# Performance work log

Hardware: AMD Instinct MI355X
Metric: run time of the kernel (lower is better)

The kernel has to match this reference:

```python
import jax, jax.numpy as jnp
import numpy as np

B, N, NS, D, H = 32, 4096, 16, 512, 8
DH = D // H          # dims_per_head = 64
DFF = 4 * D          # ff_mlp hidden
SCALE = DH ** -0.5
EPS = 1e-8           # slot-attention renorm eps
LN_EPS = 1e-5        # torch LayerNorm default
ITERS = 3


def layer_norm(x, g, b):
    mu = jnp.mean(x, axis=-1, keepdims=True)
    var = jnp.mean((x - mu) ** 2, axis=-1, keepdims=True)
    return (x - mu) * jax.lax.rsqrt(var + LN_EPS) * g + b


def setup_inputs() -> dict:
    key = jax.random.key(0)
    ks = jax.random.split(key, 8)
    s = 0.02
    return {
        "inputs": jax.random.normal(ks[0], (B, N, D), jnp.float32),
        "conditioning": jax.random.normal(ks[1], (B, NS, D), jnp.float32),
        # norm_input
        "ln_in_g": jnp.ones((D,), jnp.float32),
        "ln_in_b": jnp.zeros((D,), jnp.float32),
        # projections (no bias: use_projection_bias=False)
        "Wk": jax.random.normal(ks[2], (D, D), jnp.float32) * s,
        "Wv": jax.random.normal(ks[3], (D, D), jnp.float32) * s,
        "Wq": jax.random.normal(ks[4], (D, D), jnp.float32) * s,
        "Wo": jax.random.normal(ks[5], (D, D), jnp.float32) * s,
        # norm_slots / norm_slots_ff_mlp
        "ln_s_g": jnp.ones((D,), jnp.float32),
        "ln_s_b": jnp.zeros((D,), jnp.float32),
        "ln_f_g": jnp.ones((D,), jnp.float32),
        "ln_f_b": jnp.zeros((D,), jnp.float32),
        # ff_mlp: Linear(D,4D) -> ReLU -> Linear(4D,D)
        "W1": jax.random.normal(ks[6], (D, DFF), jnp.float32) * s,
        "b1": jnp.zeros((DFF,), jnp.float32),
        "W2": jax.random.normal(ks[7], (DFF, D), jnp.float32) * s,
        "b2": jnp.zeros((D,), jnp.float32),
    }


def reference(inputs, conditioning, ln_in_g, ln_in_b, Wk, Wv, Wq, Wo,
              ln_s_g, ln_s_b, ln_f_g, ln_f_b, W1, b1, W2, b2):
    b = inputs.shape[0]
    x = layer_norm(inputs, ln_in_g, ln_in_b)                 # [b, n, D]
    k = (x @ Wk.T).reshape(b, N, H, DH)                      # [b, n, h, dh]
    v = (x @ Wv.T).reshape(b, N, H, DH)

    slots = conditioning
    attn_mean = None
    for _ in range(ITERS):
        slots_prev = slots
        s = layer_norm(slots, ln_s_g, ln_s_b)
        q = (s @ Wq.T).reshape(b, NS, H, DH)                 # [b, ns, h, dh]
        dots = jnp.einsum("bihd,bjhd->bihj", q, k) * SCALE   # [b, ns, h, n]
        # softmax over flattened (slots, heads) axis, per input location j
        attn = jax.nn.softmax(dots.reshape(b, NS * H, N), axis=1)
        attn = attn.reshape(b, NS, H, N)
        attn_before = attn
        attn = attn + EPS
        attn = attn / jnp.sum(attn, axis=-1, keepdims=True)  # renorm over j
        updates = jnp.einsum("bjhd,bihj->bihd", v, attn)     # [b, ns, h, dh]
        updates = updates.reshape(b, NS, D)
        slots = updates @ Wo.T + slots_prev                  # to_o + residual
        slots_prev_ff = slots
        s2 = layer_norm(slots, ln_f_g, ln_f_b)
        s2 = jax.nn.relu(s2 @ W1 + b1) @ W2 + b2             # ff_mlp
        slots = s2 + slots_prev_ff
        attn_mean = jnp.mean(attn_before, axis=2)            # [b, ns, n]
    return slots, attn_mean
```

## Files before the change

kernel.cpp:

```cpp
#include <hip/hip_runtime.h>
#include <cstdint>
#include <cstddef>

typedef __attribute__((ext_vector_type(8))) short short8;
typedef __attribute__((ext_vector_type(4))) short short4v;
typedef __attribute__((ext_vector_type(8))) __bf16 bf16x8;
typedef __attribute__((ext_vector_type(4))) float f32x4;
typedef unsigned short u16;

static constexpr int Bb = 32, Nn = 4096, NSs = 16, Dd = 512, Hh = 8, DFF = 2048;
static constexpr float SCALE = 0.125f;
static constexpr float EPSR  = 1e-8f;
static constexpr float LN_EPS = 1e-5f;

__device__ __forceinline__ u16 f2b(float x) {
  union { float f; uint32_t u; } a; a.f = x;
  uint32_t r = a.u + 0x7fffu + ((a.u >> 16) & 1u);
  return (u16)(r >> 16);
}

__device__ __forceinline__ f32x4 mfma16(short8 a, short8 b, f32x4 c) {
  return __builtin_amdgcn_mfma_f32_16x16x32_bf16(
      __builtin_bit_cast(bf16x8, a), __builtin_bit_cast(bf16x8, b), c, 0, 0, 0);
}

__device__ __forceinline__ void gload16(const u16* g, u16* l) {
  __builtin_amdgcn_global_load_lds(
      (const __attribute__((address_space(1))) void*)g,
      (__attribute__((address_space(3))) void*)l, 16, 0, 0);
}

__global__ __launch_bounds__(256) void ln_rows(const float* __restrict__ src,
    const float* __restrict__ g, const float* __restrict__ bt,
    u16* __restrict__ dst, int R) {
  int row = blockIdx.x * 4 + (threadIdx.x >> 6);
  if (row >= R) return;
  int lane = threadIdx.x & 63;
  const float* p = src + (size_t)row * Dd + lane * 8;
  float4 u0 = *(const float4*)p;
  float4 u1 = *(const float4*)(p + 4);
  float x[8] = {u0.x,u0.y,u0.z,u0.w,u1.x,u1.y,u1.z,u1.w};
  float s = 0.f, s2 = 0.f;
#pragma unroll
  for (int e = 0; e < 8; ++e) { s += x[e]; s2 += x[e]*x[e]; }
#pragma unroll
  for (int m = 1; m < 64; m <<= 1) { s += __shfl_xor(s, m); s2 += __shfl_xor(s2, m); }
  float mean = s * (1.f/512.f);
  float var  = s2 * (1.f/512.f) - mean*mean;
  float rstd = rsqrtf(var + LN_EPS);
  union { u16 o[8]; short8 v; } ou;
#pragma unroll
  for (int e = 0; e < 8; ++e)
    ou.o[e] = f2b((x[e]-mean)*rstd*g[lane*8+e] + bt[lane*8+e]);
  *(short8*)(dst + (size_t)row * Dd + lane * 8) = ou.v;
}

__global__ __launch_bounds__(256, 2) void gemm_kv(const u16* __restrict__ A,
    const u16* __restrict__ Bk, const u16* __restrict__ Bv,
    u16* __restrict__ Ck, u16* __restrict__ CvT) {
  __shared__ u16 lA[2][128*32];
  __shared__ u16 lK[2][128*32];
  __shared__ u16 lV[2][128*32];
  const int tid = threadIdx.x, lane = tid & 63, wid = tid >> 6;
  const int wr = wid >> 1, wc = wid & 1;
  const int n  = blockIdx.y * 4 + blockIdx.x;
  const int orig = (n & 7) * 512 + (n >> 3);
  const int bm = (orig >> 2) * 128, bn = (orig & 3) * 128;
  const size_t BN = (size_t)Bb * Nn;
  f32x4 ak[4][4] = {};
  f32x4 av[4][4] = {};
  const int srow = wid*16 + (lane >> 2);
  const int scol = ((lane & 3) ^ ((lane >> 3) & 3)) * 8;
  const u16* Ap = A  + (size_t)(bm + srow) * Dd + scol;
  const u16* Kp = Bk + (size_t)(bn + srow) * Dd + scol;
  const u16* Vp = Bv + (size_t)(bn + srow) * Dd + scol;
  const int ldb = wid * 512;
  const int li = lane & 15, lk = lane >> 4;
  const int csw = (lk ^ ((li >> 1) & 3)) * 8;
#define KV_STAGE(buf, k0) do { \
    gload16(Ap + (k0), &lA[buf][ldb]); \
    gload16(Ap + (size_t)64*Dd + (k0), &lA[buf][ldb + 2048]); \
    gload16(Kp + (k0), &lK[buf][ldb]); \
    gload16(Kp + (size_t)64*Dd + (k0), &lK[buf][ldb + 2048]); \
    gload16(Vp + (k0), &lV[buf][ldb]); \
    gload16(Vp + (size_t)64*Dd + (k0), &lV[buf][ldb + 2048]); \
  } while (0)
  KV_STAGE(0, 0);
  int cur = 0;
  for (int t = 0; t < 16; ++t) {
    if (t < 15) {
      KV_STAGE(cur ^ 1, (t + 1) * 32);
      asm volatile("s_waitcnt vmcnt(6)" ::: "memory");
    } else {
      asm volatile("s_waitcnt vmcnt(0)" ::: "memory");
    }
    __builtin_amdgcn_sched_barrier(0);
    __builtin_amdgcn_s_barrier();
    __builtin_amdgcn_sched_barrier(0);
    short8 af[4], kf[4], vf[4];
#pragma unroll
    for (int m = 0; m < 4; ++m)
      af[m] = *(const short8*)&lA[cur][(wr*64 + m*16 + li)*32 + csw];
#pragma unroll
    for (int nn2 = 0; nn2 < 4; ++nn2) {
      kf[nn2] = *(const short8*)&lK[cur][(wc*64 + nn2*16 + li)*32 + csw];
      vf[nn2] = *(const short8*)&lV[cur][(wc*64 + nn2*16 + li)*32 + csw];
    }
    __builtin_amdgcn_s_setprio(1);
#pragma unroll
    for (int m = 0; m < 4; ++m)
#pragma unroll
      for (int nn2 = 0; nn2 < 4; ++nn2) {
        ak[m][nn2] = mfma16(af[m], kf[nn2], ak[m][nn2]);
        av[m][nn2] = mfma16(af[m], vf[nn2], av[m][nn2]);
      }
    __builtin_amdgcn_s_setprio(0);
    __builtin_amdgcn_sched_barrier(0);
    __builtin_amdgcn_s_barrier();
    __builtin_amdgcn_sched_barrier(0);
    cur ^= 1;
  }
#undef KV_STAGE
  const int lr = lk * 4;
#pragma unroll
  for (int m = 0; m < 4; ++m)
#pragma unroll
    for (int nn2 = 0; nn2 < 4; ++nn2) {
      int row = bm + wr*64 + m*16 + lr;
      int col = bn + wc*64 + nn2*16 + li;
      f32x4 vk = ak[m][nn2];
#pragma unroll
      for (int r = 0; r < 4; ++r)
        Ck[(size_t)(row + r) * Dd + col] = f2b(vk[r]);
      f32x4 vv = av[m][nn2];
      union { u16 o[4]; short4v v4; } ou;
#pragma unroll
      for (int r = 0; r < 4; ++r) ou.o[r] = f2b(vv[r]);
      *(short4v*)&CvT[(size_t)col * BN + row] = ou.v4;
    }
}

template<int EP>
__global__ __launch_bounds__(256) void gemm64(const u16* __restrict__ A,
    const u16* __restrict__ Bw, void* __restrict__ Cp,
    const float* __restrict__ bias, const float* __restrict__ res,
    int N, int K) {
  __shared__ u16 lA[2][64*32];
  __shared__ u16 lB[2][64*32];
  const int tid = threadIdx.x, lane = tid & 63, wid = tid >> 6;
  const int wr = wid >> 1, wc = wid & 1;
  const int bm = blockIdx.y * 64, bn = blockIdx.x * 64;
  f32x4 acc[2][2] = {};
  const int srow = wid*16 + (lane >> 2);
  const int scol = ((lane & 3) ^ ((lane >> 3) & 3)) * 8;
  const u16* Ap = A + (size_t)(bm + srow) * K + scol;
  const u16* Bp = Bw + (size_t)(bn + srow) * K + scol;
  const int ldb = wid * 512;
  const int li = lane & 15, lk = lane >> 4;
  const int csw = (lk ^ ((li >> 1) & 3)) * 8;
  const int nsteps = K >> 5;
  gload16(Ap, &lA[0][ldb]);
  gload16(Bp, &lB[0][ldb]);
  int cur = 0;
  for (int t = 0; t < nsteps; ++t) {
    if (t + 1 < nsteps) {
      const int k0 = (t + 1) * 32;
      gload16(Ap + k0, &lA[cur ^ 1][ldb]);
      gload16(Bp + k0, &lB[cur ^ 1][ldb]);
      asm volatile("s_waitcnt vmcnt(2)" ::: "memory");
    } else {
      asm volatile("s_waitcnt vmcnt(0)" ::: "memory");
    }
    __builtin_amdgcn_sched_barrier(0);
    __builtin_amdgcn_s_barrier();
    __builtin_amdgcn_sched_barrier(0);
    short8 af[2], bf[2];
#pragma unroll
    for (int m = 0; m < 2; ++m)
      af[m] = *(const short8*)&lA[cur][(wr*32 + m*16 + li)*32 + csw];
#pragma unroll
    for (int nn2 = 0; nn2 < 2; ++nn2)
      bf[nn2] = *(const short8*)&lB[cur][(wc*32 + nn2*16 + li)*32 + csw];
    __builtin_amdgcn_s_setprio(1);
#pragma unroll
    for (int m = 0; m < 2; ++m)
#pragma unroll
      for (int nn2 = 0; nn2 < 2; ++nn2)
        acc[m][nn2] = mfma16(af[m], bf[nn2], acc[m][nn2]);
    __builtin_amdgcn_s_setprio(0);
    __builtin_amdgcn_sched_barrier(0);
    __builtin_amdgcn_s_barrier();
    __builtin_amdgcn_sched_barrier(0);
    cur ^= 1;
  }
  const int lr = lk * 4;
#pragma unroll
  for (int m = 0; m < 2; ++m)
#pragma unroll
    for (int nn2 = 0; nn2 < 2; ++nn2) {
      int row = bm + wr*32 + m*16 + lr;
      int col = bn + wc*32 + nn2*16 + li;
      f32x4 v = acc[m][nn2];
#pragma unroll
      for (int r = 0; r < 4; ++r) {
        size_t off = (size_t)(row + r) * N + col;
        float x = v[r];
        if constexpr (EP == 0) ((u16*)Cp)[off] = f2b(x);
        else if constexpr (EP == 1) ((float*)Cp)[off] = x + res[off];
        else if constexpr (EP == 2) { x += bias[col]; ((u16*)Cp)[off] = f2b(x > 0.f ? x : 0.f); }
        else ((float*)Cp)[off] = x + bias[col] + res[off];
      }
    }
}

__global__ __launch_bounds__(256) void attn_a(const u16* __restrict__ q,
    const u16* __restrict__ kk, u16* __restrict__ attnb,
    float* __restrict__ rowsum, float* __restrict__ attn_mean) {
  const int jt = blockIdx.x, b = blockIdx.y;
  const int tid = threadIdx.x, lane = tid & 63, wid = tid >> 6;
  __shared__ float sc[64][129];
  __shared__ float red[4][64];
  const int li = lane & 15, lk = lane >> 4;
#pragma unroll
  for (int hh = 0; hh < 2; ++hh) {
    const int h = wid * 2 + hh;
    const u16* qb = q + (((size_t)b*16 + li)*8 + h)*64 + lk*8;
    short8 a0 = *(const short8*)qb;
    short8 a1 = *(const short8*)(qb + 32);
#pragma unroll
    for (int n = 0; n < 4; ++n) {
      const u16* kb = kk + ((size_t)b*Nn + jt*64 + n*16 + li)*Dd + h*64 + lk*8;
      f32x4 acc = {};
      acc = mfma16(a0, *(const short8*)kb, acc);
      acc = mfma16(a1, *(const short8*)(kb + 32), acc);
#pragma unroll
      for (int r = 0; r < 4; ++r)
        sc[n*16 + li][(lk*4 + r)*8 + h] = acc[r] * SCALE;
    }
  }
  __syncthreads();
  const int jl = tid & 63, qt = tid >> 6;
  float mx = -1e30f;
#pragma unroll
  for (int e = 0; e < 32; ++e) mx = fmaxf(mx, sc[jl][qt*32 + e]);
  red[qt][jl] = mx;
  __syncthreads();
  float M = fmaxf(fmaxf(red[0][jl], red[1][jl]), fmaxf(red[2][jl], red[3][jl]));
  __syncthreads();
  float s = 0.f;
#pragma unroll
  for (int e = 0; e < 32; ++e) {
    float ev = __expf(sc[jl][qt*32 + e] - M);
    sc[jl][qt*32 + e] = ev; s += ev;
  }
  red[qt][jl] = s;
  __syncthreads();
  float S = red[0][jl] + red[1][jl] + red[2][jl] + red[3][jl];
  float inv = 1.f / S;
#pragma unroll
  for (int e = 0; e < 32; ++e)
    sc[jl][qt*32 + e] = sc[jl][qt*32 + e] * inv + EPSR;
  __syncthreads();
  if (tid < 128) {
    float rs = 0.f;
    for (int j2 = 0; j2 < 64; ++j2) rs += sc[j2][tid];
    atomicAdd(&rowsum[b*128 + tid], rs);
  }
#pragma unroll
  for (int e = 0; e < 32; ++e) {
    int r = qt*32 + e;
    attnb[((size_t)b*128 + r)*Nn + jt*64 + jl] = f2b(sc[jl][r]);
  }
  if (attn_mean != nullptr && tid < 64) {
    for (int i = 0; i < 16; ++i) {
      float sm = 0.f;
#pragma unroll
      for (int h = 0; h < 8; ++h) sm += sc[tid][i*8 + h];
      attn_mean[((size_t)b*16 + i)*Nn + jt*64 + tid] = sm * 0.125f - EPSR;
    }
  }
}

__global__ __launch_bounds__(256) void attn_b(const u16* __restrict__ attnb,
    const u16* __restrict__ vT, float* __restrict__ Tpart) {
  const int h = blockIdx.x, js = blockIdx.y, b = blockIdx.z;
  const int lane = threadIdx.x & 63, wid = threadIdx.x >> 6;
  const int li = lane & 15, lk = lane >> 4;
  const size_t BN = (size_t)Bb * Nn;
  const int j0 = js * 1024;
  const u16* Ap = attnb + ((size_t)b*128 + li*8 + h)*Nn + j0 + lk*8;
  const u16* Bp = vT + (size_t)(h*64 + wid*16 + li)*BN + (size_t)b*Nn + j0 + lk*8;
  f32x4 acc[4] = {};
  for (int k0 = 0; k0 < 1024; k0 += 128) {
#pragma unroll
    for (int e = 0; e < 4; ++e)
      acc[e] = mfma16(*(const short8*)(Ap + k0 + e*32),
                      *(const short8*)(Bp + k0 + e*32), acc[e]);
  }
  float* Tout = Tpart + ((((size_t)js * Bb + b) * 8 + h) * 16) * 64;
#pragma unroll
  for (int r = 0; r < 4; ++r) {
    int i = lk*4 + r;
    float t = acc[0][r] + acc[1][r] + acc[2][r] + acc[3][r];
    Tout[(size_t)i * 64 + wid*16 + li] = t;
  }
}

__global__ void upd_c(const float* __restrict__ Tpart,
    const float* __restrict__ rs, u16* __restrict__ updb) {
  int idx = blockIdx.x * 256 + threadIdx.x;
  int o = idx & 511, bi = idx >> 9;
  int b = bi >> 4, i = bi & 15;
  int h = o >> 6, d = o & 63;
  size_t base = (((size_t)b * 8 + h) * 16 + i) * 64 + d;
  const size_t stride = (size_t)Bb * 8 * 16 * 64;
  float t = Tpart[base] + Tpart[base + stride]
          + Tpart[base + 2*stride] + Tpart[base + 3*stride];
  updb[idx] = f2b(t / rs[b * 128 + i * 8 + h]);
}

__global__ void cvt_w(const float* __restrict__ s, u16* __restrict__ d, int n) {
  int i = blockIdx.x*256 + threadIdx.x;
  if (i < n) d[i] = f2b(s[i]);
}
__global__ __launch_bounds__(256) void tr_cvt(const float* __restrict__ s,
    u16* __restrict__ d, int R, int C) {
  __shared__ u16 t[32][33];
  const int c0 = blockIdx.x*32, r0 = blockIdx.y*32;
  const int tr = threadIdx.x >> 3, tc4 = (threadIdx.x & 7)*4;
  float4 v = *(const float4*)&s[(size_t)(r0+tr)*C + c0 + tc4];
  t[tr][tc4+0] = f2b(v.x); t[tr][tc4+1] = f2b(v.y);
  t[tr][tc4+2] = f2b(v.z); t[tr][tc4+3] = f2b(v.w);
  __syncthreads();
  const int oc = threadIdx.x >> 3, or4 = (threadIdx.x & 7)*4;
  union { u16 o[4]; short4v v4; } ou;
#pragma unroll
  for (int e = 0; e < 4; ++e) ou.o[e] = t[or4+e][oc];
  *(short4v*)&d[(size_t)(c0+oc)*R + r0 + or4] = ou.v4;
}
__global__ void copy_f32v4(const float* __restrict__ s, float* __restrict__ d, int n4) {
  int i = blockIdx.x*256 + threadIdx.x;
  if (i < n4) ((float4*)d)[i] = ((const float4*)s)[i];
}

extern "C" void kernel_launch(void* const* d_in, const int* in_sizes, int n_in,
                              void* d_out, int out_size, void* d_ws, size_t ws_size,
                              hipStream_t stream) {
  (void)in_sizes; (void)n_in; (void)out_size; (void)ws_size;
  const float* inputs  = (const float*)d_in[0];
  const float* cond    = (const float*)d_in[1];
  const float* ln_in_g = (const float*)d_in[2];
  const float* ln_in_b = (const float*)d_in[3];
  const float* Wk = (const float*)d_in[4];
  const float* Wv = (const float*)d_in[5];
  const float* Wq = (const float*)d_in[6];
  const float* Wo = (const float*)d_in[7];
  const float* ln_s_g = (const float*)d_in[8];
  const float* ln_s_b = (const float*)d_in[9];
  const float* ln_f_g = (const float*)d_in[10];
  const float* ln_f_b = (const float*)d_in[11];
  const float* W1 = (const float*)d_in[12];
  const float* b1 = (const float*)d_in[13];
  const float* W2 = (const float*)d_in[14];
  const float* b2 = (const float*)d_in[15];
  float* out_slots = (float*)d_out;
  float* out_amean = (float*)d_out + (size_t)Bb*NSs*Dd;

  char* w = (char*)d_ws;
  auto alloc = [&](size_t bytes) {
    char* p = w; w += (bytes + 255) & ~(size_t)255; return p;
  };
  u16*  xn    = (u16*)alloc((size_t)Bb*Nn*Dd*2);
  u16*  kbuf  = (u16*)alloc((size_t)Bb*Nn*Dd*2);
  u16*  vT    = (u16*)alloc((size_t)Bb*Nn*Dd*2);
  u16*  attnb = (u16*)alloc((size_t)Bb*128*Nn*2);
  float* Tpart = (float*)alloc((size_t)4*Bb*8*16*64*4);
  float* slots = (float*)alloc((size_t)Bb*NSs*Dd*4);
  u16*  qb    = (u16*)alloc((size_t)Bb*NSs*Dd*2);
  u16*  snb   = (u16*)alloc((size_t)Bb*NSs*Dd*2);
  u16*  s2nb  = (u16*)alloc((size_t)Bb*NSs*Dd*2);
  u16*  h1b   = (u16*)alloc((size_t)Bb*NSs*DFF*2);
  u16*  updb  = (u16*)alloc((size_t)Bb*NSs*Dd*2);
  float* rowsum = (float*)alloc((size_t)Bb*128*3*4);
  u16*  wkb = (u16*)alloc(262144*2);
  u16*  wvb = (u16*)alloc(262144*2);
  u16*  wqb = (u16*)alloc(262144*2);
  u16*  wob = (u16*)alloc(262144*2);
  u16*  w1t = (u16*)alloc((size_t)1048576*2);
  u16*  w2t = (u16*)alloc((size_t)1048576*2);

  cvt_w<<<1024, 256, 0, stream>>>(Wk, wkb, 262144);
  cvt_w<<<1024, 256, 0, stream>>>(Wv, wvb, 262144);
  cvt_w<<<1024, 256, 0, stream>>>(Wq, wqb, 262144);
  cvt_w<<<1024, 256, 0, stream>>>(Wo, wob, 262144);
  tr_cvt<<<dim3(64, 16), 256, 0, stream>>>(W1, w1t, 512, 2048);
  tr_cvt<<<dim3(16, 64), 256, 0, stream>>>(W2, w2t, 2048, 512);
  copy_f32v4<<<256, 256, 0, stream>>>(cond, slots, 65536);
  (void)hipMemsetAsync(rowsum, 0, (size_t)Bb*128*3*4, stream);
  ln_rows<<<Bb*Nn/4, 256, 0, stream>>>(inputs, ln_in_g, ln_in_b, xn, Bb*Nn);
  gemm_kv<<<dim3(4, Bb*Nn/128), 256, 0, stream>>>(xn, wkb, wvb, kbuf, vT);

  for (int it = 0; it < 3; ++it) {
    float* rsp = rowsum + (size_t)it * Bb * 128;
    ln_rows<<<128, 256, 0, stream>>>(slots, ln_s_g, ln_s_b, snb, Bb*NSs);
    gemm64<0><<<dim3(8, 8), 256, 0, stream>>>(snb, wqb, qb, nullptr, nullptr, 512, 512);
    attn_a<<<dim3(Nn/64, Bb), 256, 0, stream>>>(qb, kbuf, attnb, rsp,
                                                it == 2 ? out_amean : nullptr);
    attn_b<<<dim3(Hh, 4, Bb), 256, 0, stream>>>(attnb, vT, Tpart);
    upd_c<<<1024, 256, 0, stream>>>(Tpart, rsp, updb);
    gemm64<1><<<dim3(8, 8), 256, 0, stream>>>(updb, wob, slots, nullptr, slots, 512, 512);
    ln_rows<<<128, 256, 0, stream>>>(slots, ln_f_g, ln_f_b, s2nb, Bb*NSs);
    gemm64<2><<<dim3(32, 8), 256, 0, stream>>>(s2nb, w1t, h1b, b1, nullptr, 2048, 512);
    gemm64<3><<<dim3(8, 8), 256, 0, stream>>>(h1b, w2t, slots, b2, slots, 512, 2048);
  }
  copy_f32v4<<<256, 256, 0, stream>>>(slots, out_slots, 65536);
}
```

Measured before the change: 705.9 us.

## Enlarge K/V projection GEMM tiles to 256 rows with 512 threads and BK=64

The fused K/V projection GEMM now uses 512-thread blocks covering 256 rows of normalized input by 128 columns of both K and V. The K-step is 64 with a new XOR swizzle, and the prefetch distance grows to two stages. Each block reuses its weight tiles across twice as many rows, and there are half as many barriers per K. In exchange the block needs much more LDS (about 128 KB double-buffered), which can limit occupancy, and the grid is reshaped to 2048 one-dimensional blocks.

```diff
diff --git a/kernel.cpp b/kernel.cpp
--- a/kernel.cpp
+++ b/kernel.cpp
@@ -55,69 +55,81 @@
   *(short8*)(dst + (size_t)row * Dd + lane * 8) = ou.v;
 }
 
-__global__ __launch_bounds__(256, 2) void gemm_kv(const u16* __restrict__ A,
+__global__ __launch_bounds__(512, 2) void gemm_kv(const u16* __restrict__ A,
     const u16* __restrict__ Bk, const u16* __restrict__ Bv,
     u16* __restrict__ Ck, u16* __restrict__ CvT) {
-  __shared__ u16 lA[2][128*32];
-  __shared__ u16 lK[2][128*32];
-  __shared__ u16 lV[2][128*32];
+  __shared__ u16 lA[2][256*64];
+  __shared__ u16 lK[2][128*64];
+  __shared__ u16 lV[2][128*64];
   const int tid = threadIdx.x, lane = tid & 63, wid = tid >> 6;
   const int wr = wid >> 1, wc = wid & 1;
-  const int n  = blockIdx.y * 4 + blockIdx.x;
-  const int orig = (n & 7) * 512 + (n >> 3);
-  const int bm = (orig >> 2) * 128, bn = (orig & 3) * 128;
+  const int n  = blockIdx.x;
+  const int orig = (n & 7) * 256 + (n >> 3);
+  const int bm = (orig >> 2) * 256, bn = (orig & 3) * 128;
   const size_t BN = (size_t)Bb * Nn;
   f32x4 ak[4][4] = {};
   f32x4 av[4][4] = {};
-  const int srow = wid*16 + (lane >> 2);
-  const int scol = ((lane & 3) ^ ((lane >> 3) & 3)) * 8;
-  const u16* Ap = A  + (size_t)(bm + srow) * Dd + scol;
-  const u16* Kp = Bk + (size_t)(bn + srow) * Dd + scol;
-  const u16* Vp = Bv + (size_t)(bn + srow) * Dd + scol;
-  const int ldb = wid * 512;
+  const int srow = tid >> 3;
+  const int sg = ((tid & 7) ^ (srow & 7)) * 8;
+  const u16* Ap = A  + (size_t)(bm + srow) * Dd + sg;
+  const u16* Kp = Bk + (size_t)(bn + srow) * Dd + sg;
+  const u16* Vp = Bv + (size_t)(bn + srow) * Dd + sg;
+  const int wb = wid * 8 * 64;
   const int li = lane & 15, lk = lane >> 4;
-  const int csw = (lk ^ ((li >> 1) & 3)) * 8;
-#define KV_STAGE(buf, k0) do { \
-    gload16(Ap + (k0), &lA[buf][ldb]); \
-    gload16(Ap + (size_t)64*Dd + (k0), &lA[buf][ldb + 2048]); \
-    gload16(Kp + (k0), &lK[buf][ldb]); \
-    gload16(Kp + (size_t)64*Dd + (k0), &lK[buf][ldb + 2048]); \
-    gload16(Vp + (k0), &lV[buf][ldb]); \
-    gload16(Vp + (size_t)64*Dd + (k0), &lV[buf][ldb + 2048]); \
+#define KV_STAGE(buf, t) do { const int k0 = (t) * 64; \
+    gload16(Ap + k0,                  &lA[buf][wb]); \
+    gload16(Ap + (size_t) 64*Dd + k0, &lA[buf][ 64*64 + wb]); \
+    gload16(Ap + (size_t)128*Dd + k0, &lA[buf][128*64 + wb]); \
+    gload16(Ap + (size_t)192*Dd + k0, &lA[buf][192*64 + wb]); \
+    gload16(Kp + k0,                  &lK[buf][wb]); \
+    gload16(Kp + (size_t) 64*Dd + k0, &lK[buf][ 64*64 + wb]); \
+    gload16(Vp + k0,                  &lV[buf][wb]); \
+    gload16(Vp + (size_t) 64*Dd + k0, &lV[buf][ 64*64 + wb]); \
   } while (0)
   KV_STAGE(0, 0);
+  KV_STAGE(1, 1);
+  asm volatile("s_waitcnt vmcnt(8)" ::: "memory");
+  __builtin_amdgcn_sched_barrier(0);
+  __builtin_amdgcn_s_barrier();
+  __builtin_amdgcn_sched_barrier(0);
   int cur = 0;
-  for (int t = 0; t < 16; ++t) {
-    if (t < 15) {
-      KV_STAGE(cur ^ 1, (t + 1) * 32);
-      asm volatile("s_waitcnt vmcnt(6)" ::: "memory");
-    } else {
-      asm volatile("s_waitcnt vmcnt(0)" ::: "memory");
+  for (int t = 0; t < 8; ++t) {
+#pragma unroll
+    for (int ks = 0; ks < 2; ++ks) {
+      short8 af[4], kf[4], vf[4];
+#pragma unroll
+      for (int m = 0; m < 4; ++m) {
+        const int r = wr*64 + m*16 + li;
+        af[m] = *(const short8*)&lA[cur][r*64 + (((ks*4 + lk) ^ (li & 7)) * 8)];
+      }
+#pragma unroll
+      for (int nn2 = 0; nn2 < 4; ++nn2) {
+        const int r = wc*64 + nn2*16 + li;
+        const int cs = r*64 + (((ks*4 + lk) ^ (li & 7)) * 8);
+        kf[nn2] = *(const short8*)&lK[cur][cs];
+        vf[nn2] = *(const short8*)&lV[cur][cs];
+      }
+      __builtin_amdgcn_s_setprio(1);
+#pragma unroll
+      for (int m = 0; m < 4; ++m)
+#pragma unroll
+        for (int nn2 = 0; nn2 < 4; ++nn2) {
+          ak[m][nn2] = mfma16(af[m], kf[nn2], ak[m][nn2]);
+          av[m][nn2] = mfma16(af[m], vf[nn2], av[m][nn2]);
+        }
+      __builtin_amdgcn_s_setprio(0);
     }
     __builtin_amdgcn_sched_barrier(0);
     __builtin_amdgcn_s_barrier();
     __builtin_amdgcn_sched_barrier(0);
-    short8 af[4], kf[4], vf[4];
-#pragma unroll
-    for (int m = 0; m < 4; ++m)
-      af[m] = *(const short8*)&lA[cur][(wr*64 + m*16 + li)*32 + csw];
-#pragma unroll
-    for (int nn2 = 0; nn2 < 4; ++nn2) {
-      kf[nn2] = *(const short8*)&lK[cur][(wc*64 + nn2*16 + li)*32 + csw];
-      vf[nn2] = *(const short8*)&lV[cur][(wc*64 + nn2*16 + li)*32 + csw];
-    }
-    __builtin_amdgcn_s_setprio(1);
-#pragma unroll
-    for (int m = 0; m < 4; ++m)
-#pragma unroll
-      for (int nn2 = 0; nn2 < 4; ++nn2) {
-        ak[m][nn2] = mfma16(af[m], kf[nn2], ak[m][nn2]);
-        av[m][nn2] = mfma16(af[m], vf[nn2], av[m][nn2]);
-      }
-    __builtin_amdgcn_s_setprio(0);
-    __builtin_amdgcn_sched_barrier(0);
-    __builtin_amdgcn_s_barrier();
-    __builtin_amdgcn_sched_barrier(0);
+    if (t + 2 < 8) KV_STAGE(cur, t + 2);
+    if (t < 7) {
+      if (t + 2 < 8) asm volatile("s_waitcnt vmcnt(8)" ::: "memory");
+      else           asm volatile("s_waitcnt vmcnt(0)" ::: "memory");
+      __builtin_amdgcn_sched_barrier(0);
+      __builtin_amdgcn_s_barrier();
+      __builtin_amdgcn_sched_barrier(0);
+    }
     cur ^= 1;
   }
 #undef KV_STAGE
@@ -398,7 +410,7 @@
   copy_f32v4<<<256, 256, 0, stream>>>(cond, slots, 65536);
   (void)hipMemsetAsync(rowsum, 0, (size_t)Bb*128*3*4, stream);
   ln_rows<<<Bb*Nn/4, 256, 0, stream>>>(inputs, ln_in_g, ln_in_b, xn, Bb*Nn);
-  gemm_kv<<<dim3(4, Bb*Nn/128), 256, 0, stream>>>(xn, wkb, wvb, kbuf, vT);
+  gemm_kv<<<2048, 512, 0, stream>>>(xn, wkb, wvb, kbuf, vT);
 
   for (int it = 0; it < 3; ++it) {
     float* rsp = rowsum + (size_t)it * Bb * 128;
```

Result: no change. 707.6 us (+0.2%).
